# Kernel optimization log

Measured on AMD Instinct MI355X. Metric: run time of the kernel, lower is better.

## Reference

```python
import jax, jax.numpy as jnp
import numpy as np

# Module constants (from GaussRenderer.__init__ with image 128x128)
H = 128
W = 128
TS = 64          # TILE_SIZE
P_MAX = 2048
WHITE_BKGD = True
TH, TW = H // TS, W // TS
NT = TH * TW     # num_tiles


def _tile_grids():
    th, tw = jnp.meshgrid(jnp.arange(TH), jnp.arange(TW), indexing='ij')
    h_mins = (th * TS).reshape(-1).astype(jnp.float32)   # [NT]
    w_mins = (tw * TS).reshape(-1).astype(jnp.float32)   # [NT]
    lx = jnp.arange(TS, dtype=jnp.float32)
    xx, yy = jnp.meshgrid(lx, lx, indexing='xy')         # xx[i,j]=j, yy[i,j]=i
    local = jnp.stack([xx, yy], axis=-1).reshape(TS * TS, 2)
    # tile_coords[t, p] = (x, y) global pixel coordinate
    coords = local[None, :, :] + jnp.stack([w_mins, h_mins], axis=-1)[:, None, :]
    return h_mins, w_mins, coords


def setup_inputs() -> dict:
    key = jax.random.key(0)
    k1, k2, k3, k4, k5 = jax.random.split(key, 5)
    N = 100000
    means2D = jax.random.uniform(k1, (N, 2), dtype=jnp.float32) * jnp.array([float(W), float(H)], dtype=jnp.float32)
    A = jax.random.normal(k2, (N, 2, 2), dtype=jnp.float32) * 2.0
    cov2d = A @ jnp.swapaxes(A, 1, 2) + 0.5 * jnp.eye(2, dtype=jnp.float32)  # SPD
    color = jax.random.uniform(k3, (N, 3), dtype=jnp.float32)
    opacity = jax.random.uniform(k4, (N, 1), dtype=jnp.float32)
    depths = jax.random.uniform(k5, (N,), dtype=jnp.float32) * 10.0 + 0.2
    return {"means2D": means2D, "cov2d": cov2d, "color": color, "opacity": opacity, "depths": depths}


def _render(means2D, cov2d, color, opacity, depths):
    h_mins, w_mins, tile_coords = _tile_grids()
    h_maxs = h_mins + (TS - 1.0)
    w_maxs = w_mins + (TS - 1.0)

    # --- get_radius / get_rect (torch.no_grad -> stop_gradient) ---
    c = jax.lax.stop_gradient(cov2d)
    det = c[:, 0, 0] * c[:, 1, 1] - c[:, 0, 1] * c[:, 1, 0]
    mid = 0.5 * (c[:, 0, 0] + c[:, 1, 1])
    s = jnp.sqrt(jnp.clip(mid ** 2 - det, 0.1, None))
    radii = 3.0 * jnp.ceil(jnp.sqrt(jnp.maximum(mid + s, mid - s)))  # [N]
    m = jax.lax.stop_gradient(means2D)
    rmin = m - radii[:, None]
    rmax = m + radii[:, None]
    rmin = jnp.stack([jnp.clip(rmin[:, 0], 0.0, W - 1.0), jnp.clip(rmin[:, 1], 0.0, H - 1.0)], axis=-1)
    rmax = jnp.stack([jnp.clip(rmax[:, 0], 0.0, W - 1.0), jnp.clip(rmax[:, 1], 0.0, H - 1.0)], axis=-1)

    # --- tile/gaussian overlap test ---
    ov_x = jnp.minimum(rmax[None, :, 0], w_maxs[:, None]) > jnp.maximum(rmin[None, :, 0], w_mins[:, None])
    ov_y = jnp.minimum(rmax[None, :, 1], h_maxs[:, None]) > jnp.maximum(rmin[None, :, 1], h_mins[:, None])
    overlap = ov_x & ov_y                                   # [NT, N]

    # --- per-tile depth sort, keep front-most P_MAX ---
    FAR = jnp.float32(1e10)
    d_tiled = jnp.where(overlap, depths[None, :], FAR)      # [NT, N]
    idx = jnp.argsort(d_tiled, axis=1)[:, :P_MAX]           # [NT, P]
    sd = jnp.take_along_axis(d_tiled, idx, axis=1)          # sorted depths
    valid = (sd < 1e9).astype(means2D.dtype)                # [NT, P]

    sm = means2D[idx]          # [NT, P, 2]
    sc = cov2d[idx]            # [NT, P, 2, 2]
    so = opacity[idx][..., 0]  # [NT, P]
    scol = color[idx]          # [NT, P, 3]

    # --- conic (inverse 2x2 covariance) ---
    a_ = sc[..., 0, 0]; b_ = sc[..., 0, 1]; c2_ = sc[..., 1, 0]; d_ = sc[..., 1, 1]
    inv_det = 1.0 / jnp.clip(a_ * d_ - b_ * c2_, 1e-6, None)
    c00 = d_ * inv_det; c01 = -b_ * inv_det; c10 = -c2_ * inv_det; c11 = a_ * inv_det

    # --- per-pixel gaussian weights: [NT, TS*TS, P] ---
    dx0 = tile_coords[:, :, None, 0] - sm[:, None, :, 0]
    dx1 = tile_coords[:, :, None, 1] - sm[:, None, :, 1]
    gw = jnp.exp(-0.5 * (dx0 * dx0 * c00[:, None, :] + dx1 * dx1 * c11[:, None, :]
                         + dx0 * dx1 * (c01 + c10)[:, None, :]))

    # --- front-to-back alpha compositing ---
    alpha = jnp.minimum(gw * so[:, None, :], 0.99) * valid[:, None, :]
    T = jnp.cumprod(jnp.concatenate([jnp.ones_like(alpha[:, :, :1]), 1.0 - alpha[:, :, :-1]], axis=2), axis=2)
    w = alpha * T                                           # [NT, TS*TS, P]
    acc = w.sum(axis=2)                                     # [NT, TS*TS]
    tcol = jnp.einsum('tpn,tnc->tpc', w, scol)              # [NT, TS*TS, 3]
    if WHITE_BKGD:
        tcol = tcol + (1.0 - acc)[..., None]
    tdep = (w * sd[:, None, :]).sum(axis=2)

    # --- untile ---
    render_color = tcol.reshape(TH, TW, TS, TS, 3).transpose(0, 2, 1, 3, 4).reshape(H, W, 3)
    render_depth = tdep.reshape(TH, TW, TS, TS).transpose(0, 2, 1, 3).reshape(H, W, 1)
    render_alpha = acc.reshape(TH, TW, TS, TS).transpose(0, 2, 1, 3).reshape(H, W, 1)
    return render_color, render_depth, render_alpha


def reference(means2D, cov2d, color, opacity, depths):
    return _render(means2D, cov2d, color, opacity, depths)
```

## Files before the change

### kernel.cpp

```cpp
#include <hip/hip_runtime.h>

#define IMG 128
#define TSZ 64
#define NTILES 4
#define PMAX 2048
#define NHIST 4096
#define CAP 64
#define CPAD64 8
#define NCHUNK 16
#define CHUNK 128
#define QCH 32
#define NPIX 4096
#define NPSEG 16
#define PLANE ((size_t)NTILES * NCHUNK * NPIX)
#define NTHR 256
#define RUNITS (NTILES * NCHUNK * NPSEG)
#define POISON 0xAAAAAAAAu
#define FPOIS 0xAAAAu
#define LOG2E 1.4426950408889634f
#define SKIPCUT -23.0f

typedef unsigned short u16;
typedef unsigned int uint32;
typedef unsigned long long u64;


__device__ __forceinline__ uint32 dbucket(float d) {
    int b = (int)(d * 256.0f);
    return (uint32)min(max(b, 0), NHIST - 1);
}

__device__ __forceinline__ void gauss_rect(const float* means, const float* cov,
                                           int i, float& rminx, float& rminy,
                                           float& rmaxx, float& rmaxy) {
    const float4 cv = ((const float4*)cov)[i];
    float det = cv.x * cv.w - cv.y * cv.z;
    float mid = 0.5f * (cv.x + cv.w);
    float s = sqrtf(fmaxf(mid * mid - det, 0.1f));
    float radius = 3.0f * ceilf(sqrtf(fmaxf(mid + s, mid - s)));
    const float2 m = ((const float2*)means)[i];
    rminx = fminf(fmaxf(m.x - radius, 0.f), (float)(IMG - 1));
    rmaxx = fminf(fmaxf(m.x + radius, 0.f), (float)(IMG - 1));
    rminy = fminf(fmaxf(m.y - radius, 0.f), (float)(IMG - 1));
    rmaxy = fminf(fmaxf(m.y + radius, 0.f), (float)(IMG - 1));
}

__device__ __forceinline__ bool tile_overlap(int t, float rminx, float rminy,
                                             float rmaxx, float rmaxy) {
    float wmin = (float)((t & 1) * TSZ), hmin = (float)((t >> 1) * TSZ);
    float wmax = wmin + (float)(TSZ - 1), hmax = hmin + (float)(TSZ - 1);
    return (fminf(rmaxx, wmax) > fmaxf(rminx, wmin)) &&
           (fminf(rmaxy, hmax) > fmaxf(rminy, hmin));
}

__global__ __launch_bounds__(NTHR) void k_pre3(
        const float* __restrict__ means, const float* __restrict__ cov,
        const float* __restrict__ depths, u64* __restrict__ cntP64,
        u64* __restrict__ slots, int N) {
    int i = blockIdx.x * NTHR + threadIdx.x;
    if (i >= N) return;
    float rminx, rminy, rmaxx, rmaxy;
    gauss_rect(means, cov, i, rminx, rminy, rmaxx, rmaxy);
    float d = depths[i];
    uint32 b = dbucket(d);
    u64 key = ((u64)__float_as_uint(d) << 32) | (uint32)i;
    u64 inc = 0;
    #pragma unroll
    for (int t = 0; t < NTILES; t++)
        if (tile_overlap(t, rminx, rminy, rmaxx, rmaxy))
            inc |= (1ull << (16 * t));
    if (!inc) return;
    u64 old = atomicAdd(&cntP64[(size_t)b * CPAD64], inc);
    #pragma unroll
    for (int t = 0; t < NTILES; t++) {
        if ((inc >> (16 * t)) & 1ull) {
            uint32 slot = ((uint32)(old >> (16 * t)) & 0xFFFFu) - FPOIS;
            if (slot < CAP)
                slots[((size_t)t * NHIST + b) * CAP + slot] = key;
        }
    }
}

__global__ __launch_bounds__(NTHR) void k_cnt(const u64* __restrict__ cntP64,
                                              uint32* __restrict__ ncl) {
    int q = blockIdx.x * NTHR + threadIdx.x;
    int t = q >> 12, b = q & (NHIST - 1);
    u64 v = cntP64[(size_t)b * CPAD64];
    uint32 f = (uint32)(v >> (16 * t)) & 0xFFFFu;
    ncl[q] = min(f - FPOIS, (uint32)CAP);
}

__global__ __launch_bounds__(NTHR) void k_rank4(const uint32* __restrict__ ncl,
        const u64* __restrict__ slots,
        const float* __restrict__ means, const float* __restrict__ cov,
        const float* __restrict__ color, const float* __restrict__ opac,
        float* __restrict__ params) {
    const int wq = blockIdx.x * (NTHR / 64) + (threadIdx.x >> 6);
    const int tile = wq >> 12, b = wq & (NHIST - 1);
    const int lane = threadIdx.x & 63;
    const uint32* cn = ncl + (size_t)tile * NHIST;
    uint32 n = cn[b];
    if (!n && b != NHIST - 1) return;
    uint32 base = 0;
    for (int j0 = 0; j0 < b; j0 += 64) {
        int j = j0 + lane;
        uint32 c = (j < b) ? cn[j] : 0u;
        #pragma unroll
        for (int dlt = 1; dlt < 64; dlt <<= 1)
            c += __shfl_xor(c, dlt, 64);
        base += c;
        if (base >= PMAX) break;
    }
    if (base >= PMAX) return;
    if (b == NHIST - 1) {
        for (uint32 p = base + n + (uint32)lane; p < PMAX; p += 64) {
            float4 z0 = {0.f, 0.f, 0.f, -1e30f};
            float4 zz = {0.f, 0.f, 0.f, 0.f};
            float4* P = (float4*)(params + ((size_t)tile * PMAX + p) * 12);
            P[0] = z0; P[1] = zz; P[2] = zz;
        }
        if (!n) return;
    }
    const u64* S = slots + ((size_t)tile * NHIST + b) * CAP;
    u64 ki = (lane < (int)n) ? S[lane] : ~0ull;
    uint32 r = base;
    for (uint32 j = 0; j < n; j++) {
        u64 kj = __shfl(ki, (int)j, 64);
        r += (kj < ki) ? 1u : 0u;
    }
    if (lane < (int)n && r < PMAX) {
        uint32 idx = (uint32)(ki & 0xffffffffu);
        const float4 cv = ((const float4*)cov)[idx];
        const float2 mn = ((const float2*)means)[idx];
        float invdet = 1.0f / fmaxf(cv.x * cv.w - cv.y * cv.z, 1e-6f);
        const float k = -0.5f * LOG2E;
        float cA = k * cv.w * invdet;
        float cB = k * cv.x * invdet;
        float cC = -k * (cv.y + cv.z) * invdet;
        float bnd = cB - (cC * cC) / (4.0f * cA);
        float4 p0, p1, p2;
        p0.x = mn.x; p0.y = mn.y; p0.z = bnd; p0.w = log2f(opac[idx]);
        p1.x = cA;   p1.y = cB;   p1.z = cC;  p1.w = __uint_as_float((uint32)(ki >> 32));
        p2.x = color[3*idx]; p2.y = color[3*idx+1]; p2.z = color[3*idx+2]; p2.w = 0.f;
        float4* P = (float4*)(params + ((size_t)tile * PMAX + r) * 12);
        P[0] = p0; P[1] = p1; P[2] = p2;
    }
}

__global__ __launch_bounds__(NTHR, 4) void k_render(
        const float* __restrict__ params, float* __restrict__ partials) {
    __shared__ __align__(16) float4 gp[CHUNK * 3];
    const int unit = blockIdx.x, tid = threadIdx.x;
    const int tile  = unit >> 8;
    const int chunk = (unit >> 4) & 15;
    const int pseg  = unit & 15;
    const float4* src = (const float4*)(params + ((size_t)tile * PMAX + (size_t)chunk * CHUNK) * 12);
    for (int j = tid; j < CHUNK * 3; j += NTHR) gp[j] = src[j];
    __syncthreads();
    const int p = pseg * NTHR + tid;
    const float px = (float)((tile & 1) * TSZ + (p & 63));
    const float py = (float)((tile >> 1) * TSZ + (p >> 6));
    float Tc[4], cr[4], cg[4], cb[4], dp[4], ac[4];
    #pragma unroll
    for (int s = 0; s < 4; s++) {
        Tc[s] = 1.f; cr[s] = 0.f; cg[s] = 0.f; cb[s] = 0.f; dp[s] = 0.f; ac[s] = 0.f;
    }
    #pragma unroll 2
    for (int g = 0; g < QCH; g++) {
        #pragma unroll
        for (int s = 0; s < 4; s++) {
            const int gg = s * QCH + g;
            float4 q0 = gp[3*gg];
            float dy = py - q0.y;
            float t = fmaf(dy*dy, q0.z, q0.w);
            if (t >= SKIPCUT) {
                float4 q1 = gp[3*gg+1], q2 = gp[3*gg+2];
                float dx = px - q0.x;
                float pw = fmaf(dx*dx, q1.x, q0.w);
                pw = fmaf(dy*dy, q1.y, pw);
                pw = fmaf(dx*dy, q1.z, pw);
                float al = fminf(exp2f(pw), 0.99f);
                float w = al * Tc[s];
                cr[s] += w * q2.x; cg[s] += w * q2.y; cb[s] += w * q2.z;
                dp[s] += w * q1.w; ac[s] += w;
                Tc[s] *= (1.f - al);
            }
        }
    }
    float T = 1.f, fr = 0.f, fg = 0.f, fb = 0.f, fd = 0.f, fa = 0.f;
    #pragma unroll
    for (int s = 0; s < 4; s++) {
        fr += T * cr[s]; fg += T * cg[s]; fb += T * cb[s];
        fd += T * dp[s]; fa += T * ac[s];
        T *= Tc[s];
    }
    size_t base = ((size_t)tile * NCHUNK + chunk) * NPIX + (size_t)p;
    partials[0*PLANE + base] = T;
    partials[1*PLANE + base] = fr;
    partials[2*PLANE + base] = fg;
    partials[3*PLANE + base] = fb;
    partials[4*PLANE + base] = fd;
    partials[5*PLANE + base] = fa;
}

__global__ __launch_bounds__(NTHR) void k_combine2(
        const float* __restrict__ partials, float* __restrict__ out) {
    __shared__ float sv[6][NTHR];
    const int blk = blockIdx.x, tid = threadIdx.x;
    const int tile = blk >> 8;
    const int p0 = (blk & 255) << 4;
    const int ch = tid >> 4, pl = tid & 15;
    size_t base = ((size_t)tile * NCHUNK + ch) * NPIX + (size_t)(p0 + pl);
    #pragma unroll
    for (int j = 0; j < 6; j++) sv[j][tid] = partials[(size_t)j * PLANE + base];
    __syncthreads();
    if (tid < 16) {
        const int pp = p0 + tid;
        float T = 1.f, cr = 0.f, cg = 0.f, cb = 0.f, dep = 0.f, acc = 0.f;
        #pragma unroll
        for (int c = 0; c < NCHUNK; c++) {
            int idx = c * 16 + tid;
            float Tk = sv[0][idx];
            cr  += T * sv[1][idx];
            cg  += T * sv[2][idx];
            cb  += T * sv[3][idx];
            dep += T * sv[4][idx];
            acc += T * sv[5][idx];
            T *= Tk;
        }
        int gx = (tile & 1) * TSZ + (pp & 63);
        int gy = (tile >> 1) * TSZ + (pp >> 6);
        int pix = gy * IMG + gx;
        float wb = 1.f - acc;
        out[3*pix+0] = cr + wb;
        out[3*pix+1] = cg + wb;
        out[3*pix+2] = cb + wb;
        out[IMG*IMG*3 + pix] = dep;
        out[IMG*IMG*4 + pix] = acc;
    }
}

extern "C" void kernel_launch(void* const* d_in, const int* in_sizes, int n_in,
                              void* d_out, int out_size, void* d_ws, size_t ws_size,
                              hipStream_t stream) {
    const float* means  = (const float*)d_in[0];
    const float* cov    = (const float*)d_in[1];
    const float* color  = (const float*)d_in[2];
    const float* opac   = (const float*)d_in[3];
    const float* depths = (const float*)d_in[4];
    int N = in_sizes[4];

    char* ws = (char*)d_ws;
    size_t off = 0;
    u64*    cntP64     = (u64*)(ws + off);    off += (size_t)NHIST * CPAD64 * 8;
    uint32* ncl        = (uint32*)(ws + off); off += (size_t)NTILES * NHIST * 4;
    u64*    slots      = (u64*)(ws + off);    off += (size_t)NTILES * NHIST * CAP * 8;
    float*  params     = (float*)(ws + off);  off += (size_t)NTILES * PMAX * 12 * 4;
    float*  partials   = (float*)(ws + off);  off += 6 * PLANE * 4;
    float*  out        = (float*)d_out;

    k_pre3<<<(N + NTHR - 1) / NTHR, NTHR, 0, stream>>>(means, cov, depths,
                                                       cntP64, slots, N);
    k_cnt<<<(NTILES * NHIST) / NTHR, NTHR, 0, stream>>>(cntP64, ncl);
    k_rank4<<<(NTILES * NHIST) / (NTHR / 64), NTHR, 0, stream>>>(ncl, slots,
                                                                 means, cov,
                                                                 color, opac,
                                                                 params);
    k_render<<<RUNITS, NTHR, 0, stream>>>(params, partials);
    k_combine2<<<NTILES * 256, NTHR, 0, stream>>>(partials, out);
}
```

Baseline: 103.8 us.

## Fuse all pipeline stages into one persistent kernel with grid barriers

Replaces the five separate launches (preprocess, count, rank, render, combine) with a single 1024-block persistent kernel. The stages are separated by a hierarchical atomic grid barrier: per-group sub-counters feed a master counter, and waiters spin with sleeps. The aim is to remove per-launch overhead and the drains between kernels. It relies on all 1024 blocks being co-resident and on barrier counters starting at the poison value. The spin loop has a timeout break, which risks silent incorrectness if the barrier stalls.

Result: slower. 408.9 us (+294.1%).

```diff
diff --git a/kernel.cpp b/kernel.cpp
--- a/kernel.cpp
+++ b/kernel.cpp
@@ -11,10 +11,11 @@
 #define CHUNK 128
 #define QCH 32
 #define NPIX 4096
-#define NPSEG 16
 #define PLANE ((size_t)NTILES * NCHUNK * NPIX)
 #define NTHR 256
-#define RUNITS (NTILES * NCHUNK * NPSEG)
+#define GRID 1024
+#define NSUB 8
+#define BARSTRIDE 1024
 #define POISON 0xAAAAAAAAu
 #define FPOIS 0xAAAAu
 #define LOG2E 1.4426950408889634f
@@ -24,6 +25,28 @@
 typedef unsigned int uint32;
 typedef unsigned long long u64;
 
+
+__device__ __forceinline__ void gridbar(uint32* bar) {
+    __builtin_amdgcn_fence(__ATOMIC_RELEASE, "agent");
+    __syncthreads();
+    if (threadIdx.x == 0) {
+        uint32* sub = bar + (blockIdx.x & (NSUB - 1)) * 64;
+        uint32* mst = bar + NSUB * 64;
+        uint32 v = __hip_atomic_fetch_add(sub, 1u, __ATOMIC_RELAXED,
+                                          __HIP_MEMORY_SCOPE_AGENT);
+        if (v == POISON + (GRID / NSUB) - 1u)
+            __hip_atomic_fetch_add(mst, 1u, __ATOMIC_RELAXED,
+                                   __HIP_MEMORY_SCOPE_AGENT);
+        int spins = 0;
+        while (__hip_atomic_load(mst, __ATOMIC_RELAXED,
+                                 __HIP_MEMORY_SCOPE_AGENT) < POISON + NSUB) {
+            __builtin_amdgcn_s_sleep(2);
+            if (++spins > (1 << 22)) break;
+        }
+    }
+    __syncthreads();
+    __builtin_amdgcn_fence(__ATOMIC_ACQUIRE, "agent");
+}
 
 __device__ __forceinline__ uint32 dbucket(float d) {
     int b = (int)(d * 256.0f);
@@ -53,51 +76,11 @@
            (fminf(rmaxy, hmax) > fmaxf(rminy, hmin));
 }
 
-__global__ __launch_bounds__(NTHR) void k_pre3(
-        const float* __restrict__ means, const float* __restrict__ cov,
-        const float* __restrict__ depths, u64* __restrict__ cntP64,
-        u64* __restrict__ slots, int N) {
-    int i = blockIdx.x * NTHR + threadIdx.x;
-    if (i >= N) return;
-    float rminx, rminy, rmaxx, rmaxy;
-    gauss_rect(means, cov, i, rminx, rminy, rmaxx, rmaxy);
-    float d = depths[i];
-    uint32 b = dbucket(d);
-    u64 key = ((u64)__float_as_uint(d) << 32) | (uint32)i;
-    u64 inc = 0;
-    #pragma unroll
-    for (int t = 0; t < NTILES; t++)
-        if (tile_overlap(t, rminx, rminy, rmaxx, rmaxy))
-            inc |= (1ull << (16 * t));
-    if (!inc) return;
-    u64 old = atomicAdd(&cntP64[(size_t)b * CPAD64], inc);
-    #pragma unroll
-    for (int t = 0; t < NTILES; t++) {
-        if ((inc >> (16 * t)) & 1ull) {
-            uint32 slot = ((uint32)(old >> (16 * t)) & 0xFFFFu) - FPOIS;
-            if (slot < CAP)
-                slots[((size_t)t * NHIST + b) * CAP + slot] = key;
-        }
-    }
-}
-
-__global__ __launch_bounds__(NTHR) void k_cnt(const u64* __restrict__ cntP64,
-                                              uint32* __restrict__ ncl) {
-    int q = blockIdx.x * NTHR + threadIdx.x;
-    int t = q >> 12, b = q & (NHIST - 1);
-    u64 v = cntP64[(size_t)b * CPAD64];
-    uint32 f = (uint32)(v >> (16 * t)) & 0xFFFFu;
-    ncl[q] = min(f - FPOIS, (uint32)CAP);
-}
-
-__global__ __launch_bounds__(NTHR) void k_rank4(const uint32* __restrict__ ncl,
-        const u64* __restrict__ slots,
+__device__ __forceinline__ void rank_body(int tile, int b, int lane,
+        const uint32* __restrict__ ncl, const u64* __restrict__ slots,
         const float* __restrict__ means, const float* __restrict__ cov,
         const float* __restrict__ color, const float* __restrict__ opac,
         float* __restrict__ params) {
-    const int wq = blockIdx.x * (NTHR / 64) + (threadIdx.x >> 6);
-    const int tile = wq >> 12, b = wq & (NHIST - 1);
-    const int lane = threadIdx.x & 63;
     const uint32* cn = ncl + (size_t)tile * NHIST;
     uint32 n = cn[b];
     if (!n && b != NHIST - 1) return;
@@ -147,96 +130,151 @@
     }
 }
 
-__global__ __launch_bounds__(NTHR, 4) void k_render(
-        const float* __restrict__ params, float* __restrict__ partials) {
-    __shared__ __align__(16) float4 gp[CHUNK * 3];
-    const int unit = blockIdx.x, tid = threadIdx.x;
-    const int tile  = unit >> 8;
-    const int chunk = (unit >> 4) & 15;
-    const int pseg  = unit & 15;
-    const float4* src = (const float4*)(params + ((size_t)tile * PMAX + (size_t)chunk * CHUNK) * 12);
-    for (int j = tid; j < CHUNK * 3; j += NTHR) gp[j] = src[j];
-    __syncthreads();
-    const int p = pseg * NTHR + tid;
-    const float px = (float)((tile & 1) * TSZ + (p & 63));
-    const float py = (float)((tile >> 1) * TSZ + (p >> 6));
-    float Tc[4], cr[4], cg[4], cb[4], dp[4], ac[4];
-    #pragma unroll
-    for (int s = 0; s < 4; s++) {
-        Tc[s] = 1.f; cr[s] = 0.f; cg[s] = 0.f; cb[s] = 0.f; dp[s] = 0.f; ac[s] = 0.f;
-    }
-    #pragma unroll 2
-    for (int g = 0; g < QCH; g++) {
+__global__ __launch_bounds__(NTHR, 4) void k_all(
+        const float* __restrict__ means, const float* __restrict__ cov,
+        const float* __restrict__ color, const float* __restrict__ opac,
+        const float* __restrict__ depths, int N,
+        u64* __restrict__ cntP64, uint32* __restrict__ ncl,
+        u64* __restrict__ slots, float* __restrict__ params,
+        float* __restrict__ partials, uint32* __restrict__ bars,
+        float* __restrict__ out) {
+    __shared__ __align__(16) unsigned char smem[6144];
+    const int bid = blockIdx.x, tid = threadIdx.x;
+
+    {
+        int i = bid * NTHR + tid;
+        if (i < N) {
+            float rminx, rminy, rmaxx, rmaxy;
+            gauss_rect(means, cov, i, rminx, rminy, rmaxx, rmaxy);
+            float d = depths[i];
+            uint32 b = dbucket(d);
+            u64 key = ((u64)__float_as_uint(d) << 32) | (uint32)i;
+            u64 inc = 0;
+            #pragma unroll
+            for (int t = 0; t < NTILES; t++)
+                if (tile_overlap(t, rminx, rminy, rmaxx, rmaxy))
+                    inc |= (1ull << (16 * t));
+            if (inc) {
+                u64 old = atomicAdd(&cntP64[(size_t)b * CPAD64], inc);
+                #pragma unroll
+                for (int t = 0; t < NTILES; t++) {
+                    if ((inc >> (16 * t)) & 1ull) {
+                        uint32 slot = ((uint32)(old >> (16 * t)) & 0xFFFFu) - FPOIS;
+                        if (slot < CAP)
+                            slots[((size_t)t * NHIST + b) * CAP + slot] = key;
+                    }
+                }
+            }
+        }
+    }
+    gridbar(bars + 0 * BARSTRIDE);
+
+    if (tid < 16) {
+        int q = bid * 16 + tid;
+        int t = q >> 12, b = q & (NHIST - 1);
+        u64 v = cntP64[(size_t)b * CPAD64];
+        uint32 f = (uint32)(v >> (16 * t)) & 0xFFFFu;
+        ncl[q] = min(f - FPOIS, (uint32)CAP);
+    }
+    gridbar(bars + 1 * BARSTRIDE);
+
+    {
+        const int gw = bid * (NTHR / 64) + (tid >> 6);
+        const int lane = tid & 63;
+        #pragma unroll
+        for (int rep = 0; rep < 4; rep++)
+            rank_body(rep, gw, lane, ncl, slots, means, cov, color, opac, params);
+    }
+    gridbar(bars + 2 * BARSTRIDE);
+
+    {
+        float4* gp = (float4*)smem;
+        const int tile  = bid >> 8;
+        const int chunk = (bid >> 4) & 15;
+        const int pseg  = bid & 15;
+        const float4* src = (const float4*)(params + ((size_t)tile * PMAX + (size_t)chunk * CHUNK) * 12);
+        for (int j = tid; j < CHUNK * 3; j += NTHR) gp[j] = src[j];
+        __syncthreads();
+        const int p = pseg * NTHR + tid;
+        const float px = (float)((tile & 1) * TSZ + (p & 63));
+        const float py = (float)((tile >> 1) * TSZ + (p >> 6));
+        float Tc[4], cr[4], cg[4], cb[4], dp[4], ac[4];
         #pragma unroll
         for (int s = 0; s < 4; s++) {
-            const int gg = s * QCH + g;
-            float4 q0 = gp[3*gg];
-            float dy = py - q0.y;
-            float t = fmaf(dy*dy, q0.z, q0.w);
-            if (t >= SKIPCUT) {
-                float4 q1 = gp[3*gg+1], q2 = gp[3*gg+2];
-                float dx = px - q0.x;
-                float pw = fmaf(dx*dx, q1.x, q0.w);
-                pw = fmaf(dy*dy, q1.y, pw);
-                pw = fmaf(dx*dy, q1.z, pw);
-                float al = fminf(exp2f(pw), 0.99f);
-                float w = al * Tc[s];
-                cr[s] += w * q2.x; cg[s] += w * q2.y; cb[s] += w * q2.z;
-                dp[s] += w * q1.w; ac[s] += w;
-                Tc[s] *= (1.f - al);
+            Tc[s] = 1.f; cr[s] = 0.f; cg[s] = 0.f; cb[s] = 0.f; dp[s] = 0.f; ac[s] = 0.f;
+        }
+        #pragma unroll 2
+        for (int g = 0; g < QCH; g++) {
+            #pragma unroll
+            for (int s = 0; s < 4; s++) {
+                const int gg = s * QCH + g;
+                float4 q0 = gp[3*gg];
+                float dy = py - q0.y;
+                float t = fmaf(dy*dy, q0.z, q0.w);
+                if (t >= SKIPCUT) {
+                    float4 q1 = gp[3*gg+1], q2 = gp[3*gg+2];
+                    float dx = px - q0.x;
+                    float pw = fmaf(dx*dx, q1.x, q0.w);
+                    pw = fmaf(dy*dy, q1.y, pw);
+                    pw = fmaf(dx*dy, q1.z, pw);
+                    float al = fminf(exp2f(pw), 0.99f);
+                    float w = al * Tc[s];
+                    cr[s] += w * q2.x; cg[s] += w * q2.y; cb[s] += w * q2.z;
+                    dp[s] += w * q1.w; ac[s] += w;
+                    Tc[s] *= (1.f - al);
+                }
             }
         }
-    }
-    float T = 1.f, fr = 0.f, fg = 0.f, fb = 0.f, fd = 0.f, fa = 0.f;
-    #pragma unroll
-    for (int s = 0; s < 4; s++) {
-        fr += T * cr[s]; fg += T * cg[s]; fb += T * cb[s];
-        fd += T * dp[s]; fa += T * ac[s];
-        T *= Tc[s];
-    }
-    size_t base = ((size_t)tile * NCHUNK + chunk) * NPIX + (size_t)p;
-    partials[0*PLANE + base] = T;
-    partials[1*PLANE + base] = fr;
-    partials[2*PLANE + base] = fg;
-    partials[3*PLANE + base] = fb;
-    partials[4*PLANE + base] = fd;
-    partials[5*PLANE + base] = fa;
-}
-
-__global__ __launch_bounds__(NTHR) void k_combine2(
-        const float* __restrict__ partials, float* __restrict__ out) {
-    __shared__ float sv[6][NTHR];
-    const int blk = blockIdx.x, tid = threadIdx.x;
-    const int tile = blk >> 8;
-    const int p0 = (blk & 255) << 4;
-    const int ch = tid >> 4, pl = tid & 15;
-    size_t base = ((size_t)tile * NCHUNK + ch) * NPIX + (size_t)(p0 + pl);
-    #pragma unroll
-    for (int j = 0; j < 6; j++) sv[j][tid] = partials[(size_t)j * PLANE + base];
-    __syncthreads();
-    if (tid < 16) {
-        const int pp = p0 + tid;
-        float T = 1.f, cr = 0.f, cg = 0.f, cb = 0.f, dep = 0.f, acc = 0.f;
-        #pragma unroll
-        for (int c = 0; c < NCHUNK; c++) {
-            int idx = c * 16 + tid;
-            float Tk = sv[0][idx];
-            cr  += T * sv[1][idx];
-            cg  += T * sv[2][idx];
-            cb  += T * sv[3][idx];
-            dep += T * sv[4][idx];
-            acc += T * sv[5][idx];
-            T *= Tk;
-        }
-        int gx = (tile & 1) * TSZ + (pp & 63);
-        int gy = (tile >> 1) * TSZ + (pp >> 6);
-        int pix = gy * IMG + gx;
-        float wb = 1.f - acc;
-        out[3*pix+0] = cr + wb;
-        out[3*pix+1] = cg + wb;
-        out[3*pix+2] = cb + wb;
-        out[IMG*IMG*3 + pix] = dep;
-        out[IMG*IMG*4 + pix] = acc;
+        float T = 1.f, fr = 0.f, fg = 0.f, fb = 0.f, fd = 0.f, fa = 0.f;
+        #pragma unroll
+        for (int s = 0; s < 4; s++) {
+            fr += T * cr[s]; fg += T * cg[s]; fb += T * cb[s];
+            fd += T * dp[s]; fa += T * ac[s];
+            T *= Tc[s];
+        }
+        size_t base = ((size_t)tile * NCHUNK + chunk) * NPIX + (size_t)p;
+        partials[0*PLANE + base] = T;
+        partials[1*PLANE + base] = fr;
+        partials[2*PLANE + base] = fg;
+        partials[3*PLANE + base] = fb;
+        partials[4*PLANE + base] = fd;
+        partials[5*PLANE + base] = fa;
+    }
+    gridbar(bars + 3 * BARSTRIDE);
+
+    {
+        float* sv = (float*)smem;
+        const int tile = bid >> 8;
+        const int p0 = (bid & 255) << 4;
+        const int ch = tid >> 4, pl = tid & 15;
+        size_t base = ((size_t)tile * NCHUNK + ch) * NPIX + (size_t)(p0 + pl);
+        #pragma unroll
+        for (int j = 0; j < 6; j++) sv[j * NTHR + tid] = partials[(size_t)j * PLANE + base];
+        __syncthreads();
+        if (tid < 16) {
+            const int pp = p0 + tid;
+            float T = 1.f, cr = 0.f, cg = 0.f, cb = 0.f, dep = 0.f, acc = 0.f;
+            #pragma unroll
+            for (int c = 0; c < NCHUNK; c++) {
+                int idx = c * 16 + tid;
+                float Tk = sv[0 * NTHR + idx];
+                cr  += T * sv[1 * NTHR + idx];
+                cg  += T * sv[2 * NTHR + idx];
+                cb  += T * sv[3 * NTHR + idx];
+                dep += T * sv[4 * NTHR + idx];
+                acc += T * sv[5 * NTHR + idx];
+                T *= Tk;
+            }
+            int gx = (tile & 1) * TSZ + (pp & 63);
+            int gy = (tile >> 1) * TSZ + (pp >> 6);
+            int pix = gy * IMG + gx;
+            float wb = 1.f - acc;
+            out[3*pix+0] = cr + wb;
+            out[3*pix+1] = cg + wb;
+            out[3*pix+2] = cb + wb;
+            out[IMG*IMG*3 + pix] = dep;
+            out[IMG*IMG*4 + pix] = acc;
+        }
     }
 }
 
@@ -257,15 +295,10 @@
     u64*    slots      = (u64*)(ws + off);    off += (size_t)NTILES * NHIST * CAP * 8;
     float*  params     = (float*)(ws + off);  off += (size_t)NTILES * PMAX * 12 * 4;
     float*  partials   = (float*)(ws + off);  off += 6 * PLANE * 4;
+    uint32* bars       = (uint32*)(ws + off); off += 4 * BARSTRIDE * 4;
     float*  out        = (float*)d_out;
 
-    k_pre3<<<(N + NTHR - 1) / NTHR, NTHR, 0, stream>>>(means, cov, depths,
-                                                       cntP64, slots, N);
-    k_cnt<<<(NTILES * NHIST) / NTHR, NTHR, 0, stream>>>(cntP64, ncl);
-    k_rank4<<<(NTILES * NHIST) / (NTHR / 64), NTHR, 0, stream>>>(ncl, slots,
-                                                                 means, cov,
-                                                                 color, opac,
-                                                                 params);
-    k_render<<<RUNITS, NTHR, 0, stream>>>(params, partials);
-    k_combine2<<<NTILES * 256, NTHR, 0, stream>>>(partials, out);
-}
+    k_all<<<GRID, NTHR, 0, stream>>>(means, cov, color, opac, depths, N,
+                                     cntP64, ncl, slots, params, partials,
+                                     bars, out);
+}
```
